# Kernel optimization log

Measured on AMD Instinct MI355X. Metric: run time of the kernel, lower is better.

## Reference

```python
import jax, jax.numpy as jnp
import numpy as np


def setup_inputs() -> dict:
    key = jax.random.key(0)
    k0, k1, k2, k3, k4 = jax.random.split(key, 5)
    B, C, H, W, P, M = 8, 128, 256, 256, 32, 2
    return {
        "feats": jax.random.normal(k0, (B, C, H, W), jnp.float32),
        "prototype_centers": jax.random.normal(k1, (P, C), jnp.float32) * 0.01,
        "class_membership": jax.random.uniform(k2, (P, M), jnp.float32),
        "alpha": jax.random.normal(k3, (P, 1), jnp.float32),
        # scaled so gamma^2 * d is O(1) and masses are non-degenerate
        "gamma": jax.random.uniform(k4, (P, 1), jnp.float32) * 0.2,
    }


def reference(feats, prototype_centers, class_membership, alpha, gamma):
    # feats: [B,C,H,W]; prototype_centers: [P,C]; class_membership: [P,M];
    # alpha, gamma: [P,1]. Output: normalized masses [B, M+1, H, W].
    x = feats
    Wp = prototype_centers
    BETA = class_membership
    B, C, H, Wd = x.shape
    P, M = BETA.shape

    BETA2 = BETA * BETA
    U = BETA2 / BETA2.sum(axis=1, keepdims=True)            # [P,M]
    alphap = 0.99 / (1.0 + jnp.exp(-alpha[:, 0]))            # [P]
    g2 = gamma[:, 0] ** 2                                    # [P]

    # d[p,b,h,w] = 0.5 * ||x[b,:,h,w] - W[p,:]||^2, expanded for a GEMM
    xw = jnp.einsum('bchw,pc->pbhw', x, Wp)                  # [P,B,H,W]
    x2 = 0.5 * (x * x).sum(axis=1)                           # [B,H,W]
    w2 = 0.5 * (Wp * Wp).sum(axis=1)                         # [P]
    d = x2[None] - xw + w2[:, None, None, None]              # [P,B,H,W]

    s = alphap[:, None, None, None] * jnp.exp(-g2[:, None, None, None] * d)

    # sequential Dempster-Shafer combination over prototypes (unnormalized)
    def step(carry, inputs):
        cls, om = carry                                      # [M,B,H,W], [B,H,W]
        Uk, sk = inputs                                      # [M], [B,H,W]
        mj = Uk[:, None, None, None] * sk[None]              # class masses of m_k
        mO = 1.0 - sk                                        # omega mass of m_k
        new_cls = cls * mj + cls * mO[None] + mj * om[None]
        new_om = om * mO
        return (new_cls, new_om), None

    init = (jnp.zeros((M, B, H, Wd), x.dtype), jnp.ones((B, H, Wd), x.dtype))
    (cls, om), _ = jax.lax.scan(step, init, (U, s))
    mk = jnp.concatenate([cls, om[None]], axis=0)            # [M+1,B,H,W]
    mk_n = mk / mk.sum(axis=0, keepdims=True)
    return jnp.transpose(mk_n, (1, 0, 2, 3))                 # [B,M+1,H,W]
```

## Files before the change

### kernel.cpp

```cpp
#include <hip/hip_runtime.h>

namespace {
constexpr int C = 128;
constexpr int P = 32;
constexpr int HW = 256 * 256;
constexpr int B = 8;
constexpr int PXW = 32;
constexpr int BLOCK = 256;
constexpr int PIX_PER_BLK = 4 * PXW;
constexpr int BLKS_PER_IMG = HW / PIX_PER_BLK;

typedef __attribute__((ext_vector_type(8))) short short8;
typedef __attribute__((ext_vector_type(4))) float f32x4;

__device__ inline unsigned short f2bf(float f) {
  unsigned u = __builtin_bit_cast(unsigned, f);
  return (unsigned short)((u + 0x7FFFu + ((u >> 16) & 1u)) >> 16);
}
__device__ inline unsigned pack2(float lo, float hi) {
  return (unsigned)f2bf(lo) | ((unsigned)f2bf(hi) << 16);
}

__global__ void prep_kernel(const float* __restrict__ Wp,
                            const float* __restrict__ beta,
                            const float* __restrict__ alpha,
                            const float* __restrict__ gam,
                            float* __restrict__ ws) {
  const int t = threadIdx.x;
  {
    const int p = t >> 3, seg = t & 7;
    float s = 0.f;
#pragma unroll
    for (int i = 0; i < 16; ++i) {
      const float w = Wp[p * C + seg * 16 + i];
      s = fmaf(w, w, s);
    }
#pragma unroll
    for (int m = 1; m < 8; m <<= 1) s += __shfl_xor(s, m);
    if (seg == 0) {
      ws[p] = 0.5f * s;
      ws[32 + p] = 0.99f / (1.f + __expf(-alpha[p]));
      const float gv = gam[p];
      ws[64 + p] = gv * gv;
      const float b0 = beta[p * 2 + 0], b1 = beta[p * 2 + 1];
      const float q0 = b0 * b0, q1 = b1 * b1;
      const float inv = 1.f / (q0 + q1);
      ws[96 + p] = q0 * inv;
      ws[128 + p] = q1 * inv;
    }
  }
  unsigned short* wbf = (unsigned short*)(ws + 160);
  for (int i = t; i < P * C; i += BLOCK) wbf[i] = f2bf(Wp[i]);
}

__global__ __launch_bounds__(BLOCK) void evid_kernel(const float* __restrict__ x,
                                                     const float* __restrict__ ws,
                                                     float* __restrict__ out) {
  const int t = threadIdx.x;
  const int blk = blockIdx.x;
  const int b = blk >> 9;
  const int px_blk = (blk & (BLKS_PER_IMG - 1)) * PIX_PER_BLK;
  const int wid = t >> 6, l = t & 63;
  const int li = l & 15;
  const int g = l >> 4;
  const int px_wave = px_blk + wid * PXW;
  const float* __restrict__ xg = x + (size_t)b * C * HW + px_wave + li;
  const unsigned short* __restrict__ wbf = (const unsigned short*)(ws + 160);

  f32x4 acc00 = {0.f, 0.f, 0.f, 0.f};
  f32x4 acc01 = {0.f, 0.f, 0.f, 0.f};
  f32x4 acc10 = {0.f, 0.f, 0.f, 0.f};
  f32x4 acc11 = {0.f, 0.f, 0.f, 0.f};
  float xs0 = 0.f, xs1 = 0.f;
  const int krow0 = g * 8;

#pragma unroll
  for (int s = 0; s < 4; ++s) {
    const float* xr = xg + (size_t)(s * 32 + krow0) * HW;
    float bx0[8], bx1[8];
#pragma unroll
    for (int j = 0; j < 8; ++j) {
      bx0[j] = xr[(size_t)j * HW];
      bx1[j] = xr[(size_t)j * HW + 16];
    }
    union { uint4 q; short8 v; } a0, a1;
    a0.q = *reinterpret_cast<const uint4*>(wbf + (0 * 16 + li) * C + s * 32 + krow0);
    a1.q = *reinterpret_cast<const uint4*>(wbf + (16 + li) * C + s * 32 + krow0);
    union { unsigned u[4]; short8 v; } b0, b1;
#pragma unroll
    for (int j = 0; j < 4; ++j) {
      b0.u[j] = pack2(bx0[2 * j], bx0[2 * j + 1]);
      b1.u[j] = pack2(bx1[2 * j], bx1[2 * j + 1]);
    }
#pragma unroll
    for (int j = 0; j < 8; ++j) {
      xs0 = fmaf(bx0[j], bx0[j], xs0);
      xs1 = fmaf(bx1[j], bx1[j], xs1);
    }
    acc00 = __builtin_amdgcn_mfma_f32_16x16x32_bf16(a0.v, b0.v, acc00, 0, 0, 0);
    acc01 = __builtin_amdgcn_mfma_f32_16x16x32_bf16(a1.v, b0.v, acc01, 0, 0, 0);
    acc10 = __builtin_amdgcn_mfma_f32_16x16x32_bf16(a0.v, b1.v, acc10, 0, 0, 0);
    acc11 = __builtin_amdgcn_mfma_f32_16x16x32_bf16(a1.v, b1.v, acc11, 0, 0, 0);
  }

#pragma unroll
  for (int mask = 16; mask <= 32; mask <<= 1) {
    xs0 += __shfl_xor(xs0, mask);
    xs1 += __shfl_xor(xs1, mask);
  }
  const float x2v0 = 0.5f * xs0;
  const float x2v1 = 0.5f * xs1;

  float c00 = 0.f, c01 = 0.f, om0 = 1.f;
  float c10 = 0.f, c11 = 0.f, om1 = 1.f;
#pragma unroll
  for (int r = 0; r < 4; ++r) {
#pragma unroll
    for (int T = 0; T < 2; ++T) {
      const int p = T * 16 + g * 4 + r;
      const float w2h = ws[p];
      const float ap = ws[32 + p];
      const float g2 = ws[64 + p];
      const float U0 = ws[96 + p];
      const float U1 = ws[128 + p];
      const float dot0 = (T == 0) ? acc00[r] : acc01[r];
      const float dot1 = (T == 0) ? acc10[r] : acc11[r];
      {
        const float d = x2v0 + w2h - dot0;
        const float sv = ap * __expf(-g2 * d);
        const float mO = 1.f - sv;
        const float m0 = U0 * sv, m1 = U1 * sv;
        const float n0 = fmaf(c00, m0 + mO, m0 * om0);
        const float n1 = fmaf(c01, m1 + mO, m1 * om0);
        om0 *= mO;
        c00 = n0; c01 = n1;
      }
      {
        const float d = x2v1 + w2h - dot1;
        const float sv = ap * __expf(-g2 * d);
        const float mO = 1.f - sv;
        const float m0 = U0 * sv, m1 = U1 * sv;
        const float n0 = fmaf(c10, m0 + mO, m0 * om1);
        const float n1 = fmaf(c11, m1 + mO, m1 * om1);
        om1 *= mO;
        c10 = n0; c11 = n1;
      }
    }
  }
#pragma unroll
  for (int mask = 16; mask <= 32; mask <<= 1) {
    {
      const float b0 = __shfl_xor(c00, mask);
      const float b1 = __shfl_xor(c01, mask);
      const float bO = __shfl_xor(om0, mask);
      const float n0 = c00 * b0 + c00 * bO + om0 * b0;
      const float n1 = c01 * b1 + c01 * bO + om0 * b1;
      om0 *= bO; c00 = n0; c01 = n1;
    }
    {
      const float b0 = __shfl_xor(c10, mask);
      const float b1 = __shfl_xor(c11, mask);
      const float bO = __shfl_xor(om1, mask);
      const float n0 = c10 * b0 + c10 * bO + om1 * b0;
      const float n1 = c11 * b1 + c11 * bO + om1 * b1;
      om1 *= bO; c10 = n0; c11 = n1;
    }
  }

  if (g < 2) {
    const float a = (g == 0) ? c00 : c10;
    const float bb = (g == 0) ? c01 : c11;
    const float oo = (g == 0) ? om0 : om1;
    const float inv = 1.f / (a + bb + oo);
    float* ob = out + (size_t)b * 3 * HW + px_wave + g * 16 + li;
    ob[0] = a * inv;
    ob[HW] = bb * inv;
    ob[2 * HW] = oo * inv;
  }
}
}

extern "C" void kernel_launch(void* const* d_in, const int* in_sizes, int n_in,
                              void* d_out, int out_size, void* d_ws, size_t ws_size,
                              hipStream_t stream) {
  const float* feats = (const float*)d_in[0];
  const float* Wp = (const float*)d_in[1];
  const float* beta = (const float*)d_in[2];
  const float* alpha = (const float*)d_in[3];
  const float* gam = (const float*)d_in[4];
  float* ws = (float*)d_ws;
  float* out = (float*)d_out;

  hipLaunchKernelGGL(prep_kernel, dim3(1), dim3(BLOCK), 0, stream, Wp, beta,
                     alpha, gam, ws);
  hipLaunchKernelGGL(evid_kernel, dim3(B * BLKS_PER_IMG), dim3(BLOCK), 0,
                     stream, feats, ws, out);
}
```

Before: 57.36 us.

## Vectorize pixel loads as float2, use hardware bf16 pack, parallelize prep

Each lane now owns two adjacent pixels and loads them with float2 loads instead of two strided scalar loads, so the 32-pixel wave tile maps to interleaved pixel pairs. The output stores become float2 from a single lane group and use the hardware reciprocal. Software bf16 rounding is replaced by the v_cvt_pk_bf16_f32 instruction. The prep kernel is spread over 8 blocks. Together these cut load instruction count and conversion ALU work, at the cost of slightly different reciprocal precision.

Result: faster. 51.25 us (-10.6%).

```diff
diff --git a/kernel.cpp b/kernel.cpp
--- a/kernel.cpp
+++ b/kernel.cpp
@@ -9,6 +9,7 @@
 constexpr int BLOCK = 256;
 constexpr int PIX_PER_BLK = 4 * PXW;
 constexpr int BLKS_PER_IMG = HW / PIX_PER_BLK;
+constexpr int PREP_BLKS = 8;
 
 typedef __attribute__((ext_vector_type(8))) short short8;
 typedef __attribute__((ext_vector_type(4))) float f32x4;
@@ -18,7 +19,9 @@
   return (unsigned short)((u + 0x7FFFu + ((u >> 16) & 1u)) >> 16);
 }
 __device__ inline unsigned pack2(float lo, float hi) {
-  return (unsigned)f2bf(lo) | ((unsigned)f2bf(hi) << 16);
+  unsigned r;
+  asm("v_cvt_pk_bf16_f32 %0, %1, %2" : "=v"(r) : "v"(lo), "v"(hi));
+  return r;
 }
 
 __global__ void prep_kernel(const float* __restrict__ Wp,
@@ -27,7 +30,7 @@
                             const float* __restrict__ gam,
                             float* __restrict__ ws) {
   const int t = threadIdx.x;
-  {
+  if (blockIdx.x == 0) {
     const int p = t >> 3, seg = t & 7;
     float s = 0.f;
 #pragma unroll
@@ -50,7 +53,8 @@
     }
   }
   unsigned short* wbf = (unsigned short*)(ws + 160);
-  for (int i = t; i < P * C; i += BLOCK) wbf[i] = f2bf(Wp[i]);
+  for (int i = blockIdx.x * BLOCK + t; i < P * C; i += PREP_BLKS * BLOCK)
+    wbf[i] = f2bf(Wp[i]);
 }
 
 __global__ __launch_bounds__(BLOCK) void evid_kernel(const float* __restrict__ x,
@@ -64,7 +68,7 @@
   const int li = l & 15;
   const int g = l >> 4;
   const int px_wave = px_blk + wid * PXW;
-  const float* __restrict__ xg = x + (size_t)b * C * HW + px_wave + li;
+  const float* __restrict__ xg = x + (size_t)b * C * HW + px_wave + 2 * li;
   const unsigned short* __restrict__ wbf = (const unsigned short*)(ws + 160);
 
   f32x4 acc00 = {0.f, 0.f, 0.f, 0.f};
@@ -77,30 +81,28 @@
 #pragma unroll
   for (int s = 0; s < 4; ++s) {
     const float* xr = xg + (size_t)(s * 32 + krow0) * HW;
-    float bx0[8], bx1[8];
+    float2 v[8];
 #pragma unroll
-    for (int j = 0; j < 8; ++j) {
-      bx0[j] = xr[(size_t)j * HW];
-      bx1[j] = xr[(size_t)j * HW + 16];
-    }
-    union { uint4 q; short8 v; } a0, a1;
-    a0.q = *reinterpret_cast<const uint4*>(wbf + (0 * 16 + li) * C + s * 32 + krow0);
+    for (int j = 0; j < 8; ++j)
+      v[j] = *reinterpret_cast<const float2*>(xr + (size_t)j * HW);
+    union { uint4 q; short8 s8; } a0, a1;
+    a0.q = *reinterpret_cast<const uint4*>(wbf + li * C + s * 32 + krow0);
     a1.q = *reinterpret_cast<const uint4*>(wbf + (16 + li) * C + s * 32 + krow0);
-    union { unsigned u[4]; short8 v; } b0, b1;
+    union { unsigned u[4]; short8 s8; } b0, b1;
 #pragma unroll
     for (int j = 0; j < 4; ++j) {
-      b0.u[j] = pack2(bx0[2 * j], bx0[2 * j + 1]);
-      b1.u[j] = pack2(bx1[2 * j], bx1[2 * j + 1]);
+      b0.u[j] = pack2(v[2 * j].x, v[2 * j + 1].x);
+      b1.u[j] = pack2(v[2 * j].y, v[2 * j + 1].y);
     }
 #pragma unroll
     for (int j = 0; j < 8; ++j) {
-      xs0 = fmaf(bx0[j], bx0[j], xs0);
-      xs1 = fmaf(bx1[j], bx1[j], xs1);
+      xs0 = fmaf(v[j].x, v[j].x, xs0);
+      xs1 = fmaf(v[j].y, v[j].y, xs1);
     }
-    acc00 = __builtin_amdgcn_mfma_f32_16x16x32_bf16(a0.v, b0.v, acc00, 0, 0, 0);
-    acc01 = __builtin_amdgcn_mfma_f32_16x16x32_bf16(a1.v, b0.v, acc01, 0, 0, 0);
-    acc10 = __builtin_amdgcn_mfma_f32_16x16x32_bf16(a0.v, b1.v, acc10, 0, 0, 0);
-    acc11 = __builtin_amdgcn_mfma_f32_16x16x32_bf16(a1.v, b1.v, acc11, 0, 0, 0);
+    acc00 = __builtin_amdgcn_mfma_f32_16x16x32_bf16(a0.s8, b0.s8, acc00, 0, 0, 0);
+    acc01 = __builtin_amdgcn_mfma_f32_16x16x32_bf16(a1.s8, b0.s8, acc01, 0, 0, 0);
+    acc10 = __builtin_amdgcn_mfma_f32_16x16x32_bf16(a0.s8, b1.s8, acc10, 0, 0, 0);
+    acc11 = __builtin_amdgcn_mfma_f32_16x16x32_bf16(a1.s8, b1.s8, acc11, 0, 0, 0);
   }
 
 #pragma unroll
@@ -167,15 +169,13 @@
     }
   }
 
-  if (g < 2) {
-    const float a = (g == 0) ? c00 : c10;
-    const float bb = (g == 0) ? c01 : c11;
-    const float oo = (g == 0) ? om0 : om1;
-    const float inv = 1.f / (a + bb + oo);
-    float* ob = out + (size_t)b * 3 * HW + px_wave + g * 16 + li;
-    ob[0] = a * inv;
-    ob[HW] = bb * inv;
-    ob[2 * HW] = oo * inv;
+  if (g == 0) {
+    const float inve = __builtin_amdgcn_rcpf(c00 + c01 + om0);
+    const float invo = __builtin_amdgcn_rcpf(c10 + c11 + om1);
+    float* ob = out + (size_t)b * 3 * HW + px_wave + 2 * li;
+    *reinterpret_cast<float2*>(ob) = make_float2(c00 * inve, c10 * invo);
+    *reinterpret_cast<float2*>(ob + HW) = make_float2(c01 * inve, c11 * invo);
+    *reinterpret_cast<float2*>(ob + 2 * HW) = make_float2(om0 * inve, om1 * invo);
   }
 }
 }
@@ -191,8 +191,8 @@
   float* ws = (float*)d_ws;
   float* out = (float*)d_out;
 
-  hipLaunchKernelGGL(prep_kernel, dim3(1), dim3(BLOCK), 0, stream, Wp, beta,
-                     alpha, gam, ws);
+  hipLaunchKernelGGL(prep_kernel, dim3(PREP_BLKS), dim3(BLOCK), 0, stream, Wp,
+                     beta, alpha, gam, ws);
   hipLaunchKernelGGL(evid_kernel, dim3(B * BLKS_PER_IMG), dim3(BLOCK), 0,
                      stream, feats, ws, out);
 }
```
